# Kernel optimization log

Measured on AMD Instinct MI355X. Metric: run time of the kernel, lower is better.

The kernel has to match this reference:

```python
import jax, jax.numpy as jnp
import numpy as np

N = 100000
E = 3200000
IN_C, HID_C, OUT_C = 256, 256, 128
NUM_GRAPHS = 64


def gcn_conv(x, src, dst, W, b, n_nodes):
    # PyG GCNConv: h = x @ W; out = D^{-1/2}(A+I)D^{-1/2} h + b
    loop = jnp.arange(n_nodes)
    s = jnp.concatenate([src, loop])
    d = jnp.concatenate([dst, loop])
    deg = jax.ops.segment_sum(jnp.ones_like(d, dtype=x.dtype), d, num_segments=n_nodes)
    dinv = jnp.where(deg > 0, deg ** -0.5, 0.0)
    norm = dinv[s] * dinv[d]  # [E+N]
    h = x @ W
    msg = h[s] * norm[:, None]
    out = jax.ops.segment_sum(msg, d, num_segments=n_nodes)
    return out + b


def setup_inputs() -> dict:
    key = jax.random.key(0)
    ks = jax.random.split(key, 10)
    x = jax.random.normal(ks[0], (N, IN_C), dtype=jnp.float32)
    edge_index = jax.random.randint(ks[1], (2, E), 0, N, dtype=jnp.int64)
    batch = jnp.sort(jax.random.randint(ks[2], (N,), 0, NUM_GRAPHS, dtype=jnp.int64))
    def glorot(k, fan_in, fan_out):
        lim = (6.0 / (fan_in + fan_out)) ** 0.5
        return jax.random.uniform(k, (fan_in, fan_out), jnp.float32, -lim, lim)
    return {
        "x": x,
        "edge_index": edge_index,
        "batch": batch,
        "W1": glorot(ks[3], IN_C, HID_C),
        "b1": jnp.zeros((HID_C,), jnp.float32),
        "W2": glorot(ks[4], HID_C, HID_C),
        "b2": jnp.zeros((HID_C,), jnp.float32),
        "W3": glorot(ks[5], HID_C, OUT_C),
        "b3": jnp.zeros((OUT_C,), jnp.float32),
    }


def reference(x, edge_index, batch, W1, b1, W2, b2, W3, b3):
    n = x.shape[0]
    src, dst = edge_index[0], edge_index[1]
    h = gcn_conv(x, src, dst, W1, b1, n)
    h = jax.nn.relu(h)  # dropout p=0.0 -> identity
    h = gcn_conv(h, src, dst, W2, b2, n)
    h = jax.nn.relu(h)
    h = gcn_conv(h, src, dst, W3, b3, n)
    # global_mean_pool over batch ids
    sums = jax.ops.segment_sum(h, batch, num_segments=NUM_GRAPHS)
    cnts = jax.ops.segment_sum(jnp.ones((n,), h.dtype), batch, num_segments=NUM_GRAPHS)
    return sums / jnp.maximum(cnts, 1.0)[:, None]
```

## Files before the change

kernel.cpp:

```cpp
#include <hip/hip_runtime.h>

#define IN_C 256
#define HID_C 256
#define OUT_C 128
#define NUM_GRAPHS 64
#define NBLK 256
#define NBUCK 1024

typedef _Float16 half4v __attribute__((ext_vector_type(4)));
typedef _Float16 half8v __attribute__((ext_vector_type(8)));
typedef float f32x4 __attribute__((ext_vector_type(4)));
typedef float f32x8 __attribute__((ext_vector_type(8)));


__global__ __launch_bounds__(256) void hist_kernel(const int* __restrict__ dst, int E,
                                                   int* __restrict__ ghist) {
    __shared__ int h[NBUCK];
    int tid = threadIdx.x;
#pragma unroll
    for (int j = 0; j < NBUCK / 256; ++j) h[tid + j * 256] = 0;
    __syncthreads();
    int ch = (E + NBLK - 1) / NBLK;
    int base = blockIdx.x * ch;
    int end = min(base + ch, E);
    for (int i = base + tid; i < end; i += 256)
        atomicAdd(&h[dst[i] >> 7], 1);
    __syncthreads();
#pragma unroll
    for (int j = 0; j < NBUCK / 256; ++j) {
        int b = tid + j * 256;
        ghist[b * NBLK + blockIdx.x] = h[b];
    }
}


__global__ __launch_bounds__(256) void scan_bsum_kernel(const int* __restrict__ cnt, int M,
                                                        int* __restrict__ bsum) {
    __shared__ int s[256];
    int tid = threadIdx.x;
    int i = blockIdx.x * 256 + tid;
    int v = (i < M) ? cnt[i] : 0;
    s[tid] = v;
    __syncthreads();
    for (int off = 128; off > 0; off >>= 1) {
        if (tid < off) s[tid] += s[tid + off];
        __syncthreads();
    }
    if (tid == 0) bsum[blockIdx.x] = s[0];
}

__global__ __launch_bounds__(1024) void scan_boff_kernel(const int* __restrict__ bsum, int nb,
                                                         int* __restrict__ boff) {
    __shared__ int s[1024];
    int tid = threadIdx.x;
    int v = (tid < nb) ? bsum[tid] : 0;
    s[tid] = v;
    __syncthreads();
    for (int off = 1; off < 1024; off <<= 1) {
        int t = (tid >= off) ? s[tid - off] : 0;
        __syncthreads();
        s[tid] += t;
        __syncthreads();
    }
    if (tid < nb) boff[tid] = s[tid] - v;
}

__global__ __launch_bounds__(256) void scan_write_kernel(const int* __restrict__ cnt, int M,
                                                         const int* __restrict__ boff,
                                                         int* __restrict__ S) {
    __shared__ int s[256];
    int tid = threadIdx.x;
    int i = blockIdx.x * 256 + tid;
    int v = (i < M) ? cnt[i] : 0;
    s[tid] = v;
    __syncthreads();
    for (int off = 1; off < 256; off <<= 1) {
        int t = (tid >= off) ? s[tid - off] : 0;
        __syncthreads();
        s[tid] += t;
        __syncthreads();
    }
    int incl = s[tid];
    int bo = boff[blockIdx.x];
    if (i < M) S[i] = bo + incl - v;
    if (i == M - 1) S[M] = bo + incl;
}


__global__ __launch_bounds__(256) void bucket_scatter_kernel(const int* __restrict__ src,
                                                             const int* __restrict__ dst, int E,
                                                             const int* __restrict__ S,
                                                             int2* __restrict__ sorted) {
    __shared__ int cur[NBUCK];
    int tid = threadIdx.x;
#pragma unroll
    for (int j = 0; j < NBUCK / 256; ++j) {
        int b = tid + j * 256;
        cur[b] = S[b * NBLK + blockIdx.x];
    }
    __syncthreads();
    int ch = (E + NBLK - 1) / NBLK;
    int base = blockIdx.x * ch;
    int end = min(base + ch, E);
    for (int i = base + tid; i < end; i += 256) {
        int d = dst[i], s = src[i];
        int p = atomicAdd(&cur[d >> 7], 1);
        sorted[p] = make_int2(d, s);
    }
}


__global__ __launch_bounds__(256) void bucket_csr_kernel(const int2* __restrict__ sorted,
                                                         const int* __restrict__ S,
                                                         int* __restrict__ rowptr,
                                                         int* __restrict__ csr, int N) {
    __shared__ int cnt[128], sa[128], sb[128], cur[128];
    int b = blockIdx.x;
    int tid = threadIdx.x;
    int lo = S[b << 8];
    int hi = S[(b + 1) << 8];
    if (tid < 128) cnt[tid] = 0;
    __syncthreads();
    for (int i = lo + tid; i < hi; i += 256)
        atomicAdd(&cnt[sorted[i].x & 127], 1);
    __syncthreads();
    if (tid < 128) sa[tid] = cnt[tid];
    __syncthreads();
#pragma unroll
    for (int st = 1; st < 128; st <<= 1) {
        if (tid < 128) sb[tid] = sa[tid] + ((tid >= st) ? sa[tid - st] : 0);
        __syncthreads();
        if (tid < 128) sa[tid] = sb[tid];
        __syncthreads();
    }
    if (tid < 128) {
        int offx = sa[tid] - cnt[tid];
        int idx = (b << 7) + tid;
        if (idx <= N) rowptr[idx] = lo + offx;
        cur[tid] = offx;
    }
    __syncthreads();
    for (int i = lo + tid; i < hi; i += 256) {
        int2 e = sorted[i];
        int p = atomicAdd(&cur[e.x & 127], 1);
        csr[lo + p] = e.y;
    }
}

__global__ __launch_bounds__(256) void dinv_kernel(const int* __restrict__ rowptr,
                                                   float* __restrict__ dinv, int N) {
    int i = blockIdx.x * 256 + threadIdx.x;
    if (i < N) {
        int deg = rowptr[i + 1] - rowptr[i];
        dinv[i] = rsqrtf((float)(deg + 1));
    }
}


__global__ __launch_bounds__(256) void wt_f16_kernel(const float* __restrict__ W,
                                                     _Float16* __restrict__ Wt, int K, int C) {
    int idx = blockIdx.x * 256 + threadIdx.x;
    if (idx < K * C) {
        int k = idx / C, c = idx - k * C;
        Wt[c * K + k] = (_Float16)W[idx];
    }
}


template <int BN, typename InT>
__global__ __launch_bounds__(256) void gemm_f16_kernel(const InT* __restrict__ A,
                                                       const _Float16* __restrict__ Bt,
                                                       const float* __restrict__ dinv,
                                                       _Float16* __restrict__ HS,
                                                       int nRows) {
    constexpr int K = 256;
    constexpr int BK = 32;
    constexpr int LDR = 40;
    constexpr int NF = BN / 64;

    __shared__ __align__(16) _Float16 Al[64 * LDR];
    __shared__ __align__(16) _Float16 Bl[BN * LDR];

    const int tid = threadIdx.x;
    const int wave = tid >> 6;
    const int lane = tid & 63;
    const int row0 = blockIdx.x << 6;

    const int ar = tid >> 2;
    const int ac = (tid & 3) << 3;
    const int arow = min(row0 + ar, nRows - 1);

    const int fr = lane & 15;
    const int k8 = lane >> 4;

    f32x4 acc[4][NF] = {};

    for (int k0 = 0; k0 < K; k0 += BK) {
        half8v av;
        if constexpr (sizeof(InT) == 2) {
            av = *(const half8v*)((const _Float16*)A + (size_t)arow * K + k0 + ac);
        } else {
            const float* ap = (const float*)A + (size_t)arow * K + k0 + ac;
            f32x4 lo = *(const f32x4*)(ap);
            f32x4 hi = *(const f32x4*)(ap + 4);
            half4v l = __builtin_convertvector(lo, half4v);
            half4v h = __builtin_convertvector(hi, half4v);
            av = __builtin_shufflevector(l, h, 0, 1, 2, 3, 4, 5, 6, 7);
        }
        half8v bv[NF];
#pragma unroll
        for (int j = 0; j < NF; ++j)
            bv[j] = *(const half8v*)(Bt + (size_t)(ar + 64 * j) * K + k0 + ac);
        __syncthreads();
        *(half8v*)(Al + ar * LDR + ac) = av;
#pragma unroll
        for (int j = 0; j < NF; ++j)
            *(half8v*)(Bl + (ar + 64 * j) * LDR + ac) = bv[j];
        __syncthreads();

        half8v af[4], bf[NF];
#pragma unroll
        for (int m = 0; m < 4; ++m)
            af[m] = *(const half8v*)(Al + (m * 16 + fr) * LDR + k8 * 8);
#pragma unroll
        for (int n = 0; n < NF; ++n)
            bf[n] = *(const half8v*)(Bl + (wave * (BN / 4) + n * 16 + fr) * LDR + k8 * 8);
#pragma unroll
        for (int m = 0; m < 4; ++m)
#pragma unroll
            for (int n = 0; n < NF; ++n)
                acc[m][n] = __builtin_amdgcn_mfma_f32_16x16x32_f16(af[m], bf[n], acc[m][n], 0, 0, 0);
    }

#pragma unroll
    for (int m = 0; m < 4; ++m) {
        int rb = row0 + m * 16 + k8 * 4;
        float s[4];
#pragma unroll
        for (int r = 0; r < 4; ++r) s[r] = (rb + r < nRows) ? dinv[rb + r] : 0.f;
#pragma unroll
        for (int n = 0; n < NF; ++n) {
            int col = wave * (BN / 4) + n * 16 + fr;
#pragma unroll
            for (int r = 0; r < 4; ++r) {
                int row = rb + r;
                if (row < nRows)
                    HS[(size_t)row * BN + col] = (_Float16)(acc[m][n][r] * s[r]);
            }
        }
    }
}


__global__ __launch_bounds__(256) void agg256_f16(const _Float16* __restrict__ HS,
                                                  const int* __restrict__ rowptr,
                                                  const int* __restrict__ csr,
                                                  const float* __restrict__ dinv,
                                                  const float* __restrict__ bias,
                                                  _Float16* __restrict__ OUT, int N) {
    int wid = (blockIdx.x << 2) + (threadIdx.x >> 6);
    int lane = threadIdx.x & 63;
    int v = (wid << 1) + (lane >> 5);
    if (v >= N) return;
    int co = (lane & 31) << 3;
    const _Float16* base = HS + co;

    f32x8 acc = __builtin_convertvector(*(const half8v*)(base + (size_t)v * 256), f32x8);
    f32x8 acc2 = {};
    int j = rowptr[v], end = rowptr[v + 1];
    for (; j + 2 <= end; j += 2) {
        int u0 = csr[j], u1 = csr[j + 1];
        half8v a = *(const half8v*)(base + (size_t)u0 * 256);
        half8v b = *(const half8v*)(base + (size_t)u1 * 256);
        acc  += __builtin_convertvector(a, f32x8);
        acc2 += __builtin_convertvector(b, f32x8);
    }
    if (j < end)
        acc += __builtin_convertvector(*(const half8v*)(base + (size_t)csr[j] * 256), f32x8);
    acc += acc2;

    float s = dinv[v];
    f32x4 b0 = *(const f32x4*)(bias + co);
    f32x4 b1 = *(const f32x4*)(bias + co + 4);
    f32x8 bb;
    bb.s0 = b0.x; bb.s1 = b0.y; bb.s2 = b0.z; bb.s3 = b0.w;
    bb.s4 = b1.x; bb.s5 = b1.y; bb.s6 = b1.z; bb.s7 = b1.w;
    f32x8 o = acc * s + bb;
#pragma unroll
    for (int t = 0; t < 8; ++t) o[t] = fmaxf(o[t], 0.f);
    *(half8v*)(OUT + (size_t)v * 256 + co) = __builtin_convertvector(o, half8v);
}


__global__ __launch_bounds__(256) void agg128_f16(const _Float16* __restrict__ HS,
                                                  const int* __restrict__ rowptr,
                                                  const int* __restrict__ csr,
                                                  const float* __restrict__ dinv,
                                                  const float* __restrict__ bias,
                                                  float* __restrict__ OUT, int N) {
    int wid = (blockIdx.x << 2) + (threadIdx.x >> 6);
    int lane = threadIdx.x & 63;
    int v = (wid << 2) + (lane >> 4);
    if (v >= N) return;
    int co = (lane & 15) << 3;
    const _Float16* base = HS + co;

    f32x8 acc = __builtin_convertvector(*(const half8v*)(base + (size_t)v * 128), f32x8);
    f32x8 acc2 = {};
    int j = rowptr[v], end = rowptr[v + 1];
    for (; j + 2 <= end; j += 2) {
        int u0 = csr[j], u1 = csr[j + 1];
        half8v a = *(const half8v*)(base + (size_t)u0 * 128);
        half8v b = *(const half8v*)(base + (size_t)u1 * 128);
        acc  += __builtin_convertvector(a, f32x8);
        acc2 += __builtin_convertvector(b, f32x8);
    }
    if (j < end)
        acc += __builtin_convertvector(*(const half8v*)(base + (size_t)csr[j] * 128), f32x8);
    acc += acc2;

    float s = dinv[v];
    f32x4 b0 = *(const f32x4*)(bias + co);
    f32x4 b1 = *(const f32x4*)(bias + co + 4);
    float* op = OUT + (size_t)v * 128 + co;
    f32x4 lo, hi;
    lo.x = acc.s0 * s + b0.x; lo.y = acc.s1 * s + b0.y;
    lo.z = acc.s2 * s + b0.z; lo.w = acc.s3 * s + b0.w;
    hi.x = acc.s4 * s + b1.x; hi.y = acc.s5 * s + b1.y;
    hi.z = acc.s6 * s + b1.z; hi.w = acc.s7 * s + b1.w;
    *(f32x4*)(op) = lo;
    *(f32x4*)(op + 4) = hi;
}


__global__ __launch_bounds__(64) void batch_count_kernel(const int* __restrict__ batch, int N,
                                                         int* __restrict__ gcnt) {
    int g = threadIdx.x;
    if (g >= NUM_GRAPHS) return;
    auto lb = [&](int key) {
        int lo = 0, hi = N;
        while (lo < hi) { int mid = (lo + hi) >> 1; if (batch[mid] < key) lo = mid + 1; else hi = mid; }
        return lo;
    };
    gcnt[g] = lb(g + 1) - lb(g);
}

__global__ __launch_bounds__(128) void pool_kernel(const float* __restrict__ H,
                                                   const int* __restrict__ batch,
                                                   float* __restrict__ gsum, int N) {
    const int NODES_PER_BLOCK = 256;
    int c = threadIdx.x;
    int start = blockIdx.x * NODES_PER_BLOCK;
    if (start >= N) return;
    int end = min(start + NODES_PER_BLOCK, N);
    float acc = 0.f;
    int cur = batch[start];
    for (int i = start; i < end; ++i) {
        int b = batch[i];
        if (b != cur) {
            atomicAdd(&gsum[cur * OUT_C + c], acc);
            acc = 0.f;
            cur = b;
        }
        acc += H[(size_t)i * OUT_C + c];
    }
    atomicAdd(&gsum[cur * OUT_C + c], acc);
}

__global__ __launch_bounds__(256) void finalize_kernel(const float* __restrict__ gsum,
                                                       const int* __restrict__ gcnt,
                                                       float* __restrict__ out) {
    int idx = blockIdx.x * 256 + threadIdx.x;
    if (idx < NUM_GRAPHS * OUT_C) {
        int g = idx >> 7;
        out[idx] = gsum[idx] / fmaxf((float)gcnt[g], 1.f);
    }
}


extern "C" void kernel_launch(void* const* d_in, const int* in_sizes, int n_in,
                              void* d_out, int out_size, void* d_ws, size_t ws_size,
                              hipStream_t stream) {
    const float* x  = (const float*)d_in[0];
    const int* edge = (const int*)d_in[1];
    const int* batch = (const int*)d_in[2];
    const float* W1 = (const float*)d_in[3];
    const float* b1 = (const float*)d_in[4];
    const float* W2 = (const float*)d_in[5];
    const float* b2 = (const float*)d_in[6];
    const float* W3 = (const float*)d_in[7];
    const float* b3 = (const float*)d_in[8];

    const int N = in_sizes[0] / IN_C;
    const int E = in_sizes[1] / 2;
    const int* src = edge;
    const int* dst = edge + E;
    const int M = NBUCK * NBLK;

    char* ws = (char*)d_ws;
    size_t off = 0;
    auto alloc = [&](size_t bytes) -> void* {
        void* p = ws + off;
        off += (bytes + 255) & ~(size_t)255;
        return p;
    };
    _Float16* hA   = (_Float16*)alloc((size_t)N * HID_C * sizeof(_Float16));
    _Float16* hS   = (_Float16*)alloc((size_t)N * HID_C * sizeof(_Float16));
    size_t ubytes = (size_t)N * OUT_C * sizeof(float);
    char* un      = (char*)alloc(ubytes);
    float* h3     = (float*)un;
    int2* sorted  = (int2*)un;
    int*  ghist   = (int*)(un + (size_t)E * sizeof(int2));
    int*  S       = ghist + M;
    int*  bsum    = S + M + 1;
    int*  boff    = bsum + 1024;
    _Float16* wt1  = (_Float16*)alloc((size_t)IN_C * HID_C * sizeof(_Float16));
    _Float16* wt2  = (_Float16*)alloc((size_t)HID_C * HID_C * sizeof(_Float16));
    _Float16* wt3  = (_Float16*)alloc((size_t)HID_C * OUT_C * sizeof(_Float16));
    float* dinv    = (float*)alloc((size_t)N * sizeof(float));
    int*   rowptr  = (int*)alloc((size_t)(N + 1) * sizeof(int));
    int*   csr     = (int*)alloc((size_t)E * sizeof(int));
    float* gsum    = (float*)alloc((size_t)NUM_GRAPHS * OUT_C * sizeof(float));
    int*   gcnt    = (int*)alloc((size_t)NUM_GRAPHS * sizeof(int));

    hipMemsetAsync(gsum, 0, (size_t)NUM_GRAPHS * OUT_C * sizeof(float), stream);

    int nb = (N + 255) / 256;
    int mt = (N + 63) / 64;
    int nbuck_used = (N + 127) >> 7;
    int ab256 = (((N + 1) / 2) + 3) / 4;
    int ab128 = (((N + 3) / 4) + 3) / 4;

    hist_kernel<<<NBLK, 256, 0, stream>>>(dst, E, ghist);
    scan_bsum_kernel<<<M / 256, 256, 0, stream>>>(ghist, M, bsum);
    scan_boff_kernel<<<1, 1024, 0, stream>>>(bsum, M / 256, boff);
    scan_write_kernel<<<M / 256, 256, 0, stream>>>(ghist, M, boff, S);
    bucket_scatter_kernel<<<NBLK, 256, 0, stream>>>(src, dst, E, S, sorted);
    bucket_csr_kernel<<<nbuck_used, 256, 0, stream>>>(sorted, S, rowptr, csr, N);
    dinv_kernel<<<nb, 256, 0, stream>>>(rowptr, dinv, N);
    batch_count_kernel<<<1, 64, 0, stream>>>(batch, N, gcnt);

    wt_f16_kernel<<<(IN_C * HID_C + 255) / 256, 256, 0, stream>>>(W1, wt1, IN_C, HID_C);
    wt_f16_kernel<<<(HID_C * HID_C + 255) / 256, 256, 0, stream>>>(W2, wt2, HID_C, HID_C);
    wt_f16_kernel<<<(HID_C * OUT_C + 255) / 256, 256, 0, stream>>>(W3, wt3, HID_C, OUT_C);

    gemm_f16_kernel<256, float><<<mt, 256, 0, stream>>>(x, wt1, dinv, hS, N);
    agg256_f16<<<ab256, 256, 0, stream>>>(hS, rowptr, csr, dinv, b1, hA, N);
    gemm_f16_kernel<256, _Float16><<<mt, 256, 0, stream>>>(hA, wt2, dinv, hS, N);
    agg256_f16<<<ab256, 256, 0, stream>>>(hS, rowptr, csr, dinv, b2, hA, N);
    gemm_f16_kernel<128, _Float16><<<mt, 256, 0, stream>>>(hA, wt3, dinv, hS, N);
    agg128_f16<<<ab128, 256, 0, stream>>>(hS, rowptr, csr, dinv, b3, h3, N);

    pool_kernel<<<(N + 255) / 256, 128, 0, stream>>>(h3, batch, gsum, N);
    finalize_kernel<<<(NUM_GRAPHS * OUT_C + 255) / 256, 256, 0, stream>>>(gsum, gcnt, (float*)d_out);
}
```

Measured before the change: 911.8 us.

## Pack sorted edges into 32-bit, fuse weight casts, widen GEMM tiles, fp16 final output

Bucket-sorted edges are packed into one 32-bit word (low 7 bits of dst plus a 17-bit src) instead of an int2, halving scatter and CSR-build traffic. The three weight transpose/cast launches are merged into one kernel. The 256-wide GEMMs now use 512-thread blocks covering 128 rows, so each B tile is reused across more rows. The last aggregation writes fp16 instead of fp32, halving its store and the pool read, at the cost of precision. The 17-bit packing assumes N is at most 131072.

```diff
diff --git a/kernel.cpp b/kernel.cpp
--- a/kernel.cpp
+++ b/kernel.cpp
@@ -32,7 +32,6 @@
         ghist[b * NBLK + blockIdx.x] = h[b];
     }
 }
-
 
 __global__ __launch_bounds__(256) void scan_bsum_kernel(const int* __restrict__ cnt, int M,
                                                         int* __restrict__ bsum) {
@@ -90,7 +89,7 @@
 __global__ __launch_bounds__(256) void bucket_scatter_kernel(const int* __restrict__ src,
                                                              const int* __restrict__ dst, int E,
                                                              const int* __restrict__ S,
-                                                             int2* __restrict__ sorted) {
+                                                             unsigned int* __restrict__ sorted) {
     __shared__ int cur[NBUCK];
     int tid = threadIdx.x;
 #pragma unroll
@@ -105,12 +104,12 @@
     for (int i = base + tid; i < end; i += 256) {
         int d = dst[i], s = src[i];
         int p = atomicAdd(&cur[d >> 7], 1);
-        sorted[p] = make_int2(d, s);
-    }
-}
-
-
-__global__ __launch_bounds__(256) void bucket_csr_kernel(const int2* __restrict__ sorted,
+        sorted[p] = ((unsigned int)(d & 127) << 17) | (unsigned int)s;
+    }
+}
+
+
+__global__ __launch_bounds__(256) void bucket_csr_kernel(const unsigned int* __restrict__ sorted,
                                                          const int* __restrict__ S,
                                                          int* __restrict__ rowptr,
                                                          int* __restrict__ csr, int N) {
@@ -122,7 +121,7 @@
     if (tid < 128) cnt[tid] = 0;
     __syncthreads();
     for (int i = lo + tid; i < hi; i += 256)
-        atomicAdd(&cnt[sorted[i].x & 127], 1);
+        atomicAdd(&cnt[sorted[i] >> 17], 1);
     __syncthreads();
     if (tid < 128) sa[tid] = cnt[tid];
     __syncthreads();
@@ -141,9 +140,9 @@
     }
     __syncthreads();
     for (int i = lo + tid; i < hi; i += 256) {
-        int2 e = sorted[i];
-        int p = atomicAdd(&cur[e.x & 127], 1);
-        csr[lo + p] = e.y;
+        unsigned int e = sorted[i];
+        int p = atomicAdd(&cur[e >> 17], 1);
+        csr[lo + p] = (int)(e & 0x1FFFFu);
     }
 }
 
@@ -157,43 +156,60 @@
 }
 
 
-__global__ __launch_bounds__(256) void wt_f16_kernel(const float* __restrict__ W,
-                                                     _Float16* __restrict__ Wt, int K, int C) {
+__global__ __launch_bounds__(256) void wt_all_kernel(const float* __restrict__ W1,
+                                                     const float* __restrict__ W2,
+                                                     const float* __restrict__ W3,
+                                                     _Float16* __restrict__ wt1,
+                                                     _Float16* __restrict__ wt2,
+                                                     _Float16* __restrict__ wt3) {
     int idx = blockIdx.x * 256 + threadIdx.x;
-    if (idx < K * C) {
-        int k = idx / C, c = idx - k * C;
-        Wt[c * K + k] = (_Float16)W[idx];
-    }
-}
-
-
-template <int BN, typename InT>
-__global__ __launch_bounds__(256) void gemm_f16_kernel(const InT* __restrict__ A,
-                                                       const _Float16* __restrict__ Bt,
-                                                       const float* __restrict__ dinv,
-                                                       _Float16* __restrict__ HS,
-                                                       int nRows) {
+    const int S1 = IN_C * HID_C;
+    const int S2 = S1 + HID_C * HID_C;
+    const int S3 = S2 + HID_C * OUT_C;
+    if (idx < S1) {
+        int k = idx >> 8, c = idx & 255;
+        wt1[c * IN_C + k] = (_Float16)W1[idx];
+    } else if (idx < S2) {
+        int li = idx - S1;
+        int k = li >> 8, c = li & 255;
+        wt2[c * HID_C + k] = (_Float16)W2[idx - S1];
+    } else if (idx < S3) {
+        int li = idx - S2;
+        int k = li >> 7, c = li & 127;
+        wt3[c * HID_C + k] = (_Float16)W3[li];
+    }
+}
+
+
+template <typename InT>
+__global__ __launch_bounds__(512) void gemm_f16_wide(const InT* __restrict__ A,
+                                                     const _Float16* __restrict__ Bt,
+                                                     const float* __restrict__ dinv,
+                                                     _Float16* __restrict__ HS,
+                                                     int nRows) {
     constexpr int K = 256;
     constexpr int BK = 32;
     constexpr int LDR = 40;
-    constexpr int NF = BN / 64;
-
-    __shared__ __align__(16) _Float16 Al[64 * LDR];
-    __shared__ __align__(16) _Float16 Bl[BN * LDR];
+    constexpr int BN = 256;
+
+    __shared__ __align__(16) _Float16 Al[128 * LDR];
+    __shared__ __align__(16) _Float16 Bl[256 * LDR];
 
     const int tid = threadIdx.x;
     const int wave = tid >> 6;
     const int lane = tid & 63;
-    const int row0 = blockIdx.x << 6;
+    const int row0 = blockIdx.x << 7;
 
     const int ar = tid >> 2;
     const int ac = (tid & 3) << 3;
     const int arow = min(row0 + ar, nRows - 1);
 
+    const int rh = wave >> 2;
+    const int cq = wave & 3;
     const int fr = lane & 15;
     const int k8 = lane >> 4;
 
-    f32x4 acc[4][NF] = {};
+    f32x4 acc[4][4] = {};
 
     for (int k0 = 0; k0 < K; k0 += BK) {
         half8v av;
@@ -207,6 +223,78 @@
             half4v h = __builtin_convertvector(hi, half4v);
             av = __builtin_shufflevector(l, h, 0, 1, 2, 3, 4, 5, 6, 7);
         }
+        half8v bv0 = *(const half8v*)(Bt + (size_t)ar * K + k0 + ac);
+        half8v bv1 = *(const half8v*)(Bt + (size_t)(ar + 128) * K + k0 + ac);
+        __syncthreads();
+        *(half8v*)(Al + ar * LDR + ac) = av;
+        *(half8v*)(Bl + ar * LDR + ac) = bv0;
+        *(half8v*)(Bl + (ar + 128) * LDR + ac) = bv1;
+        __syncthreads();
+
+        half8v af[4], bf[4];
+#pragma unroll
+        for (int m = 0; m < 4; ++m)
+            af[m] = *(const half8v*)(Al + (rh * 64 + m * 16 + fr) * LDR + k8 * 8);
+#pragma unroll
+        for (int n = 0; n < 4; ++n)
+            bf[n] = *(const half8v*)(Bl + (cq * 64 + n * 16 + fr) * LDR + k8 * 8);
+#pragma unroll
+        for (int m = 0; m < 4; ++m)
+#pragma unroll
+            for (int n = 0; n < 4; ++n)
+                acc[m][n] = __builtin_amdgcn_mfma_f32_16x16x32_f16(af[m], bf[n], acc[m][n], 0, 0, 0);
+    }
+
+#pragma unroll
+    for (int m = 0; m < 4; ++m) {
+        int rb = row0 + rh * 64 + m * 16 + k8 * 4;
+        float s[4];
+#pragma unroll
+        for (int r = 0; r < 4; ++r) s[r] = (rb + r < nRows) ? dinv[rb + r] : 0.f;
+#pragma unroll
+        for (int n = 0; n < 4; ++n) {
+            int col = cq * 64 + n * 16 + fr;
+#pragma unroll
+            for (int r = 0; r < 4; ++r) {
+                int row = rb + r;
+                if (row < nRows)
+                    HS[(size_t)row * BN + col] = (_Float16)(acc[m][n][r] * s[r]);
+            }
+        }
+    }
+}
+
+
+__global__ __launch_bounds__(256) void gemm_f16_128(const _Float16* __restrict__ A,
+                                                    const _Float16* __restrict__ Bt,
+                                                    const float* __restrict__ dinv,
+                                                    _Float16* __restrict__ HS,
+                                                    int nRows) {
+    constexpr int K = 256;
+    constexpr int BK = 32;
+    constexpr int LDR = 40;
+    constexpr int BN = 128;
+    constexpr int NF = 2;
+
+    __shared__ __align__(16) _Float16 Al[64 * LDR];
+    __shared__ __align__(16) _Float16 Bl[BN * LDR];
+
+    const int tid = threadIdx.x;
+    const int wave = tid >> 6;
+    const int lane = tid & 63;
+    const int row0 = blockIdx.x << 6;
+
+    const int ar = tid >> 2;
+    const int ac = (tid & 3) << 3;
+    const int arow = min(row0 + ar, nRows - 1);
+
+    const int fr = lane & 15;
+    const int k8 = lane >> 4;
+
+    f32x4 acc[4][NF] = {};
+
+    for (int k0 = 0; k0 < K; k0 += BK) {
+        half8v av = *(const half8v*)(A + (size_t)arow * K + k0 + ac);
         half8v bv[NF];
 #pragma unroll
         for (int j = 0; j < NF; ++j)
@@ -297,7 +385,7 @@
                                                   const int* __restrict__ csr,
                                                   const float* __restrict__ dinv,
                                                   const float* __restrict__ bias,
-                                                  float* __restrict__ OUT, int N) {
+                                                  _Float16* __restrict__ OUT, int N) {
     int wid = (blockIdx.x << 2) + (threadIdx.x >> 6);
     int lane = threadIdx.x & 63;
     int v = (wid << 2) + (lane >> 4);
@@ -322,14 +410,12 @@
     float s = dinv[v];
     f32x4 b0 = *(const f32x4*)(bias + co);
     f32x4 b1 = *(const f32x4*)(bias + co + 4);
-    float* op = OUT + (size_t)v * 128 + co;
-    f32x4 lo, hi;
-    lo.x = acc.s0 * s + b0.x; lo.y = acc.s1 * s + b0.y;
-    lo.z = acc.s2 * s + b0.z; lo.w = acc.s3 * s + b0.w;
-    hi.x = acc.s4 * s + b1.x; hi.y = acc.s5 * s + b1.y;
-    hi.z = acc.s6 * s + b1.z; hi.w = acc.s7 * s + b1.w;
-    *(f32x4*)(op) = lo;
-    *(f32x4*)(op + 4) = hi;
+    f32x8 o;
+    o.s0 = acc.s0 * s + b0.x; o.s1 = acc.s1 * s + b0.y;
+    o.s2 = acc.s2 * s + b0.z; o.s3 = acc.s3 * s + b0.w;
+    o.s4 = acc.s4 * s + b1.x; o.s5 = acc.s5 * s + b1.y;
+    o.s6 = acc.s6 * s + b1.z; o.s7 = acc.s7 * s + b1.w;
+    *(half8v*)(OUT + (size_t)v * 128 + co) = __builtin_convertvector(o, half8v);
 }
 
 
@@ -345,7 +431,7 @@
     gcnt[g] = lb(g + 1) - lb(g);
 }
 
-__global__ __launch_bounds__(128) void pool_kernel(const float* __restrict__ H,
+__global__ __launch_bounds__(128) void pool_kernel(const _Float16* __restrict__ H,
                                                    const int* __restrict__ batch,
                                                    float* __restrict__ gsum, int N) {
     const int NODES_PER_BLOCK = 256;
@@ -362,7 +448,7 @@
             acc = 0.f;
             cur = b;
         }
-        acc += H[(size_t)i * OUT_C + c];
+        acc += (float)H[(size_t)i * OUT_C + c];
     }
     atomicAdd(&gsum[cur * OUT_C + c], acc);
 }
@@ -406,11 +492,11 @@
     };
     _Float16* hA   = (_Float16*)alloc((size_t)N * HID_C * sizeof(_Float16));
     _Float16* hS   = (_Float16*)alloc((size_t)N * HID_C * sizeof(_Float16));
-    size_t ubytes = (size_t)N * OUT_C * sizeof(float);
+    size_t ubytes = (size_t)N * OUT_C * sizeof(_Float16);
     char* un      = (char*)alloc(ubytes);
-    float* h3     = (float*)un;
-    int2* sorted  = (int2*)un;
-    int*  ghist   = (int*)(un + (size_t)E * sizeof(int2));
+    _Float16* h3  = (_Float16*)un;
+    unsigned int* sorted = (unsigned int*)un;
+    int*  ghist   = (int*)(un + (size_t)E * sizeof(unsigned int));
     int*  S       = ghist + M;
     int*  bsum    = S + M + 1;
     int*  boff    = bsum + 1024;
@@ -426,6 +512,7 @@
     hipMemsetAsync(gsum, 0, (size_t)NUM_GRAPHS * OUT_C * sizeof(float), stream);
 
     int nb = (N + 255) / 256;
+    int mtw = (N + 127) / 128;
     int mt = (N + 63) / 64;
     int nbuck_used = (N + 127) >> 7;
     int ab256 = (((N + 1) / 2) + 3) / 4;
@@ -440,15 +527,14 @@
     dinv_kernel<<<nb, 256, 0, stream>>>(rowptr, dinv, N);
     batch_count_kernel<<<1, 64, 0, stream>>>(batch, N, gcnt);
 
-    wt_f16_kernel<<<(IN_C * HID_C + 255) / 256, 256, 0, stream>>>(W1, wt1, IN_C, HID_C);
-    wt_f16_kernel<<<(HID_C * HID_C + 255) / 256, 256, 0, stream>>>(W2, wt2, HID_C, HID_C);
-    wt_f16_kernel<<<(HID_C * OUT_C + 255) / 256, 256, 0, stream>>>(W3, wt3, HID_C, OUT_C);
-
-    gemm_f16_kernel<256, float><<<mt, 256, 0, stream>>>(x, wt1, dinv, hS, N);
+    wt_all_kernel<<<(IN_C * HID_C + HID_C * HID_C + HID_C * OUT_C + 255) / 256, 256, 0, stream>>>(
+        W1, W2, W3, wt1, wt2, wt3);
+
+    gemm_f16_wide<float><<<mtw, 512, 0, stream>>>(x, wt1, dinv, hS, N);
     agg256_f16<<<ab256, 256, 0, stream>>>(hS, rowptr, csr, dinv, b1, hA, N);
-    gemm_f16_kernel<256, _Float16><<<mt, 256, 0, stream>>>(hA, wt2, dinv, hS, N);
+    gemm_f16_wide<_Float16><<<mtw, 512, 0, stream>>>(hA, wt2, dinv, hS, N);
     agg256_f16<<<ab256, 256, 0, stream>>>(hS, rowptr, csr, dinv, b2, hA, N);
-    gemm_f16_kernel<128, _Float16><<<mt, 256, 0, stream>>>(hA, wt3, dinv, hS, N);
+    gemm_f16_128<<<mt, 256, 0, stream>>>(hA, wt3, dinv, hS, N);
     agg128_f16<<<ab128, 256, 0, stream>>>(hS, rowptr, csr, dinv, b3, h3, N);
 
     pool_kernel<<<(N + 255) / 256, 128, 0, stream>>>(h3, batch, gsum, N);
```

Result: faster. 861.2 us, median of 2 (-5.5%).
